# Kernel tuning notes

Hardware: AMD Instinct MI355X
Metric: run time of the kernel (lower is better)

The kernel has to match this reference:

```python
import jax, jax.numpy as jnp
import numpy as np

B, N, C, O, K, D = 32, 2048, 64, 64, 3, 16

def setup_inputs() -> dict:
    key = jax.random.key(0)
    ks = jax.random.split(key, 6)
    x = jax.random.normal(ks[0], (B, N, C), dtype=jnp.float32)
    node_embeddings = jax.random.normal(ks[1], (N, D), dtype=jnp.float32)
    adj_m = jax.random.uniform(ks[2], (N, N), dtype=jnp.float32)
    weights_pool = jax.random.normal(ks[3], (D, K, C, O), dtype=jnp.float32) * 0.1
    bias_pool = jax.random.normal(ks[4], (D, O), dtype=jnp.float32) * 0.1
    sa_weight = jax.random.normal(ks[5], (N, 2 * N), dtype=jnp.float32) * (1.0 / np.sqrt(2 * N))
    return {"x": x, "node_embeddings": node_embeddings, "adj_m": adj_m,
            "weights_pool": weights_pool, "bias_pool": bias_pool, "sa_weight": sa_weight}

def reference(x, node_embeddings, adj_m, weights_pool, bias_pool, sa_weight):
    n = node_embeddings.shape[0]
    # learned adaptive adjacency [N,N]
    supports = jax.nn.softmax(jax.nn.relu(node_embeddings @ node_embeddings.T), axis=1)
    # SpatialAttention: 1x1 conv over 2N channels == matmul with [N,2N] weight
    z = jnp.concatenate([supports, adj_m], axis=1) @ sa_weight.T  # [N,N]
    s2 = jax.nn.sigmoid(z)
    supports = s2 * adj_m + (1.0 - s2) * supports
    # Chebyshev polynomial basis
    support_set = [jnp.eye(n, dtype=supports.dtype), supports]
    for _ in range(2, K):
        support_set.append(2.0 * supports @ support_set[-1] - support_set[-2])
    supports_k = jnp.stack(support_set, axis=0)  # [K,N,N]
    # per-node generated weights/bias from embeddings
    weights = jnp.einsum('nd,dkio->nkio', node_embeddings, weights_pool)  # [N,K,C,O]
    bias = node_embeddings @ bias_pool  # [N,O]
    # graph conv: aggregate then per-node matmul
    x_g = jnp.einsum('knm,bmc->bnkc', supports_k, x)  # [B,N,K,C]
    x_gconv = jnp.einsum('bnki,nkio->bno', x_g, weights) + bias  # [B,N,O]
    return x_gconv
```

## Files before the change

### kernel.cpp

```cpp
#include <hip/hip_runtime.h>


typedef unsigned short u16;
typedef float f32x4 __attribute__((ext_vector_type(4)));
typedef __bf16 bf16x8 __attribute__((ext_vector_type(8)));
typedef unsigned short u16x8 __attribute__((ext_vector_type(8)));

__device__ __forceinline__ u16 f2bf(float f) {
    unsigned u = __float_as_uint(f);
    u += 0x7FFFu + ((u >> 16) & 1u);
    return (u16)(u >> 16);
}
__device__ __forceinline__ float bf2f(u16 h) {
    return __uint_as_float((unsigned)h << 16);
}
__device__ __forceinline__ void gl_lds16(const void* g, void* l) {
    __builtin_amdgcn_global_load_lds(
        (const __attribute__((address_space(1))) unsigned*)g,
        (__attribute__((address_space(3))) unsigned*)l, 16, 0, 0);
}

__global__ __launch_bounds__(256)
void supports_softmax(const float* __restrict__ E, u16* __restrict__ Acat) {
    const int n = blockIdx.x, tid = threadIdx.x;
    const int lane = tid & 63, wave = tid >> 6;
    __shared__ float red[4];
    float e[16];
#pragma unroll
    for (int d = 0; d < 16; ++d) e[d] = E[n * 16 + d];
    float v[8];
    float mx = 0.f;
#pragma unroll
    for (int r = 0; r < 8; ++r) {
        int m = r * 256 + tid;
        const float4* Er = (const float4*)(E + (size_t)m * 16);
        float4 a = Er[0], b = Er[1], c = Er[2], d4 = Er[3];
        float s = 0.f;
        s = fmaf(a.x, e[0], s);  s = fmaf(a.y, e[1], s);
        s = fmaf(a.z, e[2], s);  s = fmaf(a.w, e[3], s);
        s = fmaf(b.x, e[4], s);  s = fmaf(b.y, e[5], s);
        s = fmaf(b.z, e[6], s);  s = fmaf(b.w, e[7], s);
        s = fmaf(c.x, e[8], s);  s = fmaf(c.y, e[9], s);
        s = fmaf(c.z, e[10], s); s = fmaf(c.w, e[11], s);
        s = fmaf(d4.x, e[12], s); s = fmaf(d4.y, e[13], s);
        s = fmaf(d4.z, e[14], s); s = fmaf(d4.w, e[15], s);
        s = fmaxf(s, 0.f);
        v[r] = s;
        mx = fmaxf(mx, s);
    }
    for (int off = 32; off; off >>= 1) mx = fmaxf(mx, __shfl_down(mx, off, 64));
    if (lane == 0) red[wave] = mx;
    __syncthreads();
    mx = fmaxf(fmaxf(red[0], red[1]), fmaxf(red[2], red[3]));
    __syncthreads();
    float sum = 0.f;
#pragma unroll
    for (int r = 0; r < 8; ++r) { v[r] = __expf(v[r] - mx); sum += v[r]; }
    for (int off = 32; off; off >>= 1) sum += __shfl_down(sum, off, 64);
    if (lane == 0) red[wave] = sum;
    __syncthreads();
    sum = red[0] + red[1] + red[2] + red[3];
    float inv = 1.f / sum;
#pragma unroll
    for (int r = 0; r < 8; ++r)
        Acat[(size_t)n * 4096 + r * 256 + tid] = f2bf(v[r] * inv);
}

__global__ __launch_bounds__(256)
void cast_inputs(const float* __restrict__ adj, const float* __restrict__ saw,
                 const float* __restrict__ x, u16* __restrict__ Acat,
                 u16* __restrict__ sawb, u16* __restrict__ x_bf) {
    int bid = blockIdx.x;
    if (bid < 4096) {
        size_t j = ((size_t)bid * 256 + threadIdx.x) * 4;
        float4 v = *(const float4*)(adj + j);
        int n = (int)(j >> 11), c = (int)(j & 2047);
        ushort4 o = make_ushort4(f2bf(v.x), f2bf(v.y), f2bf(v.z), f2bf(v.w));
        *(ushort4*)(Acat + (size_t)n * 4096 + 2048 + c) = o;
    } else if (bid < 12288) {
        size_t j = ((size_t)(bid - 4096) * 256 + threadIdx.x) * 4;
        float4 v = *(const float4*)(saw + j);
        ushort4 o = make_ushort4(f2bf(v.x), f2bf(v.y), f2bf(v.z), f2bf(v.w));
        *(ushort4*)(sawb + j) = o;
    } else {
        size_t j = ((size_t)(bid - 12288) * 256 + threadIdx.x) * 4;
        float4 v = *(const float4*)(x + j);
        ushort4 o = make_ushort4(f2bf(v.x), f2bf(v.y), f2bf(v.z), f2bf(v.w));
        *(ushort4*)(x_bf + j) = o;
    }
}

__global__ __launch_bounds__(256)
void build_xtT(const float* __restrict__ x, u16* __restrict__ xtT) {
    __shared__ u16 t[64][65];
    int b = blockIdx.y, m0 = blockIdx.x * 64;
    int c = threadIdx.x & 63, g = threadIdx.x >> 6;
#pragma unroll
    for (int r = 0; r < 16; ++r) {
        int mm = g * 16 + r;
        t[mm][c] = f2bf(x[((size_t)b * 2048 + m0 + mm) * 64 + c]);
    }
    __syncthreads();
#pragma unroll
    for (int r = 0; r < 16; ++r) {
        int cc = g * 16 + r;
        xtT[((size_t)b * 64 + cc) * 2048 + m0 + c] = t[c][cc];
    }
}

__global__ __launch_bounds__(256, 3)
void gemm_bt(const u16* __restrict__ A, const u16* __restrict__ Bt,
             u16* __restrict__ Cp, int M, int N, int K, int Kh) {
    __shared__ alignas(16) u16 As[128 * 64];
    __shared__ alignas(16) u16 Bs[128 * 64];
    const int tid = threadIdx.x, lane = tid & 63, wave = tid >> 6;
    const int m0 = blockIdx.y * 128, n0 = blockIdx.x * 128;
    const int wm = (wave >> 1) * 64, wn = (wave & 1) * 64;
    const int kbeg = blockIdx.z * Kh, kend = kbeg + Kh;
    const int ml = lane & 15, c0l = lane >> 4;
    f32x4 acc[4][4] = {};

    int baseA[4], mskA[4], baseB[4], mskB[4];
#pragma unroll
    for (int i = 0; i < 4; ++i) { int m = wm + i * 16 + ml; baseA[i] = m * 8; mskA[i] = m & 7; }
#pragma unroll
    for (int j = 0; j < 4; ++j) { int nn = wn + j * 16 + ml; baseB[j] = nn * 8; mskB[j] = nn & 7; }

    for (int k0 = kbeg; k0 < kend; k0 += 64) {
#pragma unroll
        for (int r = 0; r < 4; ++r) {
            int s = wave * 64 + r * 256 + lane;
            int row = s >> 3, gc = (s & 7) ^ (row & 7);
            gl_lds16(A + (size_t)(m0 + row) * K + k0 + gc * 8, As + (size_t)s * 8);
        }
#pragma unroll
        for (int r = 0; r < 4; ++r) {
            int s = wave * 64 + r * 256 + lane;
            int row = s >> 3, gc = (s & 7) ^ (row & 7);
            gl_lds16(Bt + (size_t)(n0 + row) * K + k0 + gc * 8, Bs + (size_t)s * 8);
        }
        __syncthreads();
#pragma unroll
        for (int ks4 = 0; ks4 < 8; ks4 += 4) {
            bf16x8 af[4], bv[4];
#pragma unroll
            for (int i = 0; i < 4; ++i)
                af[i] = *(const bf16x8*)(As + (baseA[i] + ((c0l + ks4) ^ mskA[i])) * 8);
#pragma unroll
            for (int j = 0; j < 4; ++j)
                bv[j] = *(const bf16x8*)(Bs + (baseB[j] + ((c0l + ks4) ^ mskB[j])) * 8);
#pragma unroll
            for (int i = 0; i < 4; ++i)
#pragma unroll
                for (int j = 0; j < 4; ++j)
                    acc[i][j] = __builtin_amdgcn_mfma_f32_16x16x32_bf16(af[i], bv[j], acc[i][j], 0, 0, 0);
        }
        __syncthreads();
    }

    const int col_l = lane & 15, row_l = (lane >> 4) * 4;
    u16* Cz = Cp + (size_t)blockIdx.z * M * N;
#pragma unroll
    for (int i = 0; i < 4; ++i)
#pragma unroll
        for (int j = 0; j < 4; ++j)
#pragma unroll
            for (int r = 0; r < 4; ++r) {
                int row = m0 + wm + i * 16 + row_l + r;
                int col = n0 + wn + j * 16 + col_l;
                Cz[(size_t)row * N + col] = f2bf(acc[i][j][r]);
            }
}

#define PSTRIDE ((size_t)2048 * 2048)
__global__ __launch_bounds__(256)
void reduce_z(const u16* __restrict__ p, const float* __restrict__ adj,
              const u16* __restrict__ Acat, u16* __restrict__ S) {
    size_t j = ((size_t)blockIdx.x * 256 + threadIdx.x) * 4;
    ushort4 p0 = *(const ushort4*)(p + j);
    ushort4 p1 = *(const ushort4*)(p + PSTRIDE + j);
    ushort4 p2 = *(const ushort4*)(p + 2 * PSTRIDE + j);
    ushort4 p3 = *(const ushort4*)(p + 3 * PSTRIDE + j);
    float4 ad = *(const float4*)(adj + j);
    int row = (int)(j >> 11), col = (int)(j & 2047);
    ushort4 sp = *(const ushort4*)(Acat + (size_t)row * 4096 + col);
    float z0 = bf2f(p0.x) + bf2f(p1.x) + bf2f(p2.x) + bf2f(p3.x);
    float z1 = bf2f(p0.y) + bf2f(p1.y) + bf2f(p2.y) + bf2f(p3.y);
    float z2 = bf2f(p0.z) + bf2f(p1.z) + bf2f(p2.z) + bf2f(p3.z);
    float z3 = bf2f(p0.w) + bf2f(p1.w) + bf2f(p2.w) + bf2f(p3.w);
    float s0 = 1.f / (1.f + __expf(-z0)), s1 = 1.f / (1.f + __expf(-z1));
    float s2 = 1.f / (1.f + __expf(-z2)), s3 = 1.f / (1.f + __expf(-z3));
    ushort4 o = make_ushort4(
        f2bf(s0 * ad.x + (1.f - s0) * bf2f(sp.x)),
        f2bf(s1 * ad.y + (1.f - s1) * bf2f(sp.y)),
        f2bf(s2 * ad.z + (1.f - s2) * bf2f(sp.z)),
        f2bf(s3 * ad.w + (1.f - s3) * bf2f(sp.w)));
    *(ushort4*)(S + j) = o;
}

__global__ __launch_bounds__(256)
void reduceT(const u16* __restrict__ p, u16* __restrict__ xg1b,
             u16* __restrict__ xg1T) {
    __shared__ u16 t[64][65];
    int bx = blockIdx.x * 64, by = blockIdx.y * 64;
    int c = threadIdx.x & 63, g = threadIdx.x >> 6;
    int b = bx >> 6;
#pragma unroll
    for (int r = 0; r < 16; ++r) {
        int row = g * 16 + r;
        size_t idx = (size_t)(by + row) * 2048 + bx + c;
        u16 v = f2bf(bf2f(p[idx]) + bf2f(p[PSTRIDE + idx]) +
                     bf2f(p[2 * PSTRIDE + idx]) + bf2f(p[3 * PSTRIDE + idx]));
        xg1b[((size_t)b * 2048 + by + row) * 64 + c] = v;
        t[row][c] = v;
    }
    __syncthreads();
#pragma unroll
    for (int r = 0; r < 16; ++r) {
        int row = g * 16 + r;
        xg1T[(size_t)(bx + row) * 2048 + by + c] = t[c][row];
    }
}

__global__ __launch_bounds__(256)
void reduce2(const u16* __restrict__ p, u16* __restrict__ xg2b) {
    size_t j = ((size_t)blockIdx.x * 256 + threadIdx.x) * 4;
    ushort4 p0 = *(const ushort4*)(p + j);
    ushort4 p1 = *(const ushort4*)(p + PSTRIDE + j);
    ushort4 p2 = *(const ushort4*)(p + 2 * PSTRIDE + j);
    ushort4 p3 = *(const ushort4*)(p + 3 * PSTRIDE + j);
    int n = (int)(j >> 11), bc = (int)(j & 2047);
    int b = bc >> 6, c = bc & 63;
    ushort4 o = make_ushort4(
        f2bf(bf2f(p0.x) + bf2f(p1.x) + bf2f(p2.x) + bf2f(p3.x)),
        f2bf(bf2f(p0.y) + bf2f(p1.y) + bf2f(p2.y) + bf2f(p3.y)),
        f2bf(bf2f(p0.z) + bf2f(p1.z) + bf2f(p2.z) + bf2f(p3.z)),
        f2bf(bf2f(p0.w) + bf2f(p1.w) + bf2f(p2.w) + bf2f(p3.w)));
    *(ushort4*)(xg2b + ((size_t)b * 2048 + n) * 64 + c) = o;
}

__global__ __launch_bounds__(256)
void prep(const float* __restrict__ Wp, const float* __restrict__ E,
          const float* __restrict__ bp, u16* __restrict__ Wpb,
          float* __restrict__ bias) {
    const int bid = blockIdx.x, tid = threadIdx.x;
    if (bid < 16) {
        const int d = bid;
        const float* base = Wp + (size_t)d * 12288;
        for (int idx = tid; idx < 12288; idx += 256) {
            int o = idx / 192, ki = idx - o * 192;
            int k = ki >> 6, i = ki & 63;
            float v;
            if (k == 0)      v = base[i * 64 + o] - base[2 * 4096 + i * 64 + o];
            else if (k == 1) v = base[4096 + i * 64 + o];
            else             v = 2.f * base[2 * 4096 + i * 64 + o];
            Wpb[(size_t)(d * 64 + o) * 192 + ki] = f2bf(v);
        }
    } else {
        const int nb = bid - 16;
#pragma unroll
        for (int it = 0; it < 8; ++it) {
            int idx = tid + it * 256;
            int n = nb * 32 + (idx >> 6), o = idx & 63;
            float s = 0.f;
#pragma unroll
            for (int d = 0; d < 16; ++d) s = fmaf(E[n * 16 + d], bp[d * 64 + o], s);
            bias[(size_t)n * 64 + o] = s;
        }
    }
}

__global__ __launch_bounds__(256, 2)
void gconv_mfma(const u16* __restrict__ x_bf, const u16* __restrict__ xg1,
                const u16* __restrict__ xg2, const u16* __restrict__ Wpb,
                const float* __restrict__ bias, const float* __restrict__ E,
                float* __restrict__ out) {
    __shared__ alignas(16) u16 As[128 * 192];
    __shared__ alignas(16) u16 Bs[64 * 192];
    __shared__ float El[16 * 128];
    const int tid = threadIdx.x, lane = tid & 63, wave = tid >> 6;
    const int m0 = blockIdx.x * 128, nb = m0 & 2047;
    const int wm = (wave >> 1) * 64, wn = (wave & 1) * 32;
    const int ml = lane & 15, c0l = lane >> 4;
    const int col_l = lane & 15, rl = (lane >> 4) * 4;

#pragma unroll
    for (int it = 0; it < 12; ++it) {
        int s = tid + it * 256;
        int row = s / 24, sc = s - row * 24;
        int gc = (sc & 24) | ((sc ^ row) & 7);
        const u16* src = (gc < 8) ? x_bf : (gc < 16 ? xg1 : xg2);
        gl_lds16(src + (size_t)(m0 + row) * 64 + (gc & 7) * 8, As + (size_t)s * 8);
    }
#pragma unroll
    for (int it = 0; it < 8; ++it) {
        int idx = tid + it * 256;
        El[idx] = E[(size_t)(nb + (idx & 127)) * 16 + (idx >> 7)];
    }
    f32x4 oacc[4][2];
#pragma unroll
    for (int i = 0; i < 4; ++i)
#pragma unroll
        for (int j = 0; j < 2; ++j)
#pragma unroll
            for (int r = 0; r < 4; ++r)
                oacc[i][j][r] = bias[(size_t)(nb + wm + i * 16 + rl + r) * 64 + wn + j * 16 + col_l];
    __syncthreads();

    bf16x8 af[4][6];
#pragma unroll
    for (int i = 0; i < 4; ++i) {
        int m = wm + i * 16 + ml, base = m * 24, msk = m & 7;
#pragma unroll
        for (int ks = 0; ks < 6; ++ks) {
            int c = c0l + ks * 4;
            af[i][ks] = *(const bf16x8*)(As + (base + ((c & 24) | ((c ^ msk) & 7))) * 8);
        }
    }

    for (int d = 0; d < 16; ++d) {
        if (d) __syncthreads();
#pragma unroll
        for (int it = 0; it < 6; ++it) {
            int s = tid + it * 256;
            int row = s / 24, sc = s - row * 24;
            int gc = (sc & 24) | ((sc ^ row) & 7);
            gl_lds16(Wpb + (size_t)(d * 64 + row) * 192 + gc * 8, Bs + (size_t)s * 8);
        }
        __syncthreads();
        f32x4 tmp[4][2] = {};
#pragma unroll
        for (int ks = 0; ks < 6; ++ks) {
            bf16x8 bv[2];
#pragma unroll
            for (int j = 0; j < 2; ++j) {
                int o = wn + j * 16 + ml, msk = o & 7, c = c0l + ks * 4;
                bv[j] = *(const bf16x8*)(Bs + (o * 24 + ((c & 24) | ((c ^ msk) & 7))) * 8);
            }
#pragma unroll
            for (int i = 0; i < 4; ++i)
#pragma unroll
                for (int j = 0; j < 2; ++j)
                    tmp[i][j] = __builtin_amdgcn_mfma_f32_16x16x32_bf16(af[i][ks], bv[j], tmp[i][j], 0, 0, 0);
        }
#pragma unroll
        for (int i = 0; i < 4; ++i)
#pragma unroll
            for (int r = 0; r < 4; ++r) {
                float ev = El[d * 128 + wm + i * 16 + rl + r];
#pragma unroll
                for (int j = 0; j < 2; ++j)
                    oacc[i][j][r] = fmaf(ev, tmp[i][j][r], oacc[i][j][r]);
            }
    }
#pragma unroll
    for (int i = 0; i < 4; ++i)
#pragma unroll
        for (int j = 0; j < 2; ++j)
#pragma unroll
            for (int r = 0; r < 4; ++r)
                out[(size_t)(m0 + wm + i * 16 + rl + r) * 64 + wn + j * 16 + col_l] = oacc[i][j][r];
}

extern "C" void kernel_launch(void* const* d_in, const int* in_sizes, int n_in,
                              void* d_out, int out_size, void* d_ws, size_t ws_size,
                              hipStream_t stream) {
    const float* x   = (const float*)d_in[0];
    const float* E   = (const float*)d_in[1];
    const float* adj = (const float*)d_in[2];
    const float* Wp  = (const float*)d_in[3];
    const float* bp  = (const float*)d_in[4];
    const float* saw = (const float*)d_in[5];
    float* out = (float*)d_out;

    char* ws = (char*)d_ws;
    const size_t MB = 1u << 20;
    u16*   Acat  = (u16*)(ws);
    u16*   sawb  = (u16*)(ws + 16 * MB);
    u16*   XtT   = (u16*)(ws + 32 * MB);
    u16*   x_bf  = (u16*)(ws + 40 * MB);
    u16*   part  = (u16*)(ws + 48 * MB);
    u16*   S_bf  = (u16*)(ws + 16 * MB);
    u16*   xg1T  = (u16*)(ws + 24 * MB);
    u16*   xg1b  = (u16*)(ws);
    u16*   xg2b  = (u16*)(ws + 8 * MB);
    u16*   Wpb   = (u16*)(ws + 32 * MB);
    float* bias  = (float*)(ws + 33 * MB);

    supports_softmax<<<2048, 256, 0, stream>>>(E, Acat);
    cast_inputs<<<16384, 256, 0, stream>>>(adj, saw, x, Acat, sawb, x_bf);
    build_xtT<<<dim3(32, 32), 256, 0, stream>>>(x, XtT);

    gemm_bt<<<dim3(16, 16, 4), 256, 0, stream>>>(Acat, sawb, part, 2048, 2048, 4096, 1024);
    reduce_z<<<4096, 256, 0, stream>>>(part, adj, Acat, S_bf);
    gemm_bt<<<dim3(16, 16, 4), 256, 0, stream>>>(S_bf, XtT, part, 2048, 2048, 2048, 512);
    reduceT<<<dim3(32, 32), 256, 0, stream>>>(part, xg1b, xg1T);
    prep<<<80, 256, 0, stream>>>(Wp, E, bp, Wpb, bias);
    gemm_bt<<<dim3(16, 16, 4), 256, 0, stream>>>(S_bf, xg1T, part, 2048, 2048, 2048, 512);
    reduce2<<<4096, 256, 0, stream>>>(part, xg2b);

    gconv_mfma<<<512, 256, 0, stream>>>(x_bf, xg1b, xg2b, Wpb, bias, E, out);
}
```

Before: 306.2 us.

## Merge preprocessing kernels and fold split-K reduction and x cast into gconv

Merges softmax, casts, the x transpose and weight/bias prep into one preamble launch, and drops the separate x_bf cast. The reduce2 pass is removed: gconv_mfma now sums the four split-K partials and casts x to bf16 while loading its A tile, replacing async global-to-LDS loads with register loads. reduce_z reads the bf16 adjacency from Acat instead of the fp32 input, and reduceT is vectorized to ushort4 loads. The aim is fewer launches and less intermediate memory traffic, at the cost of losing the async LDS loads in gconv and using a slightly less precise adjacency blend.

```diff
diff --git a/kernel.cpp b/kernel.cpp
--- a/kernel.cpp
+++ b/kernel.cpp
@@ -6,6 +6,8 @@
 typedef __bf16 bf16x8 __attribute__((ext_vector_type(8)));
 typedef unsigned short u16x8 __attribute__((ext_vector_type(8)));
 
+#define PSTRIDE ((size_t)2048 * 2048)
+
 __device__ __forceinline__ u16 f2bf(float f) {
     unsigned u = __float_as_uint(f);
     u += 0x7FFFu + ((u >> 16) & 1u);
@@ -21,90 +23,109 @@
 }
 
 __global__ __launch_bounds__(256)
-void supports_softmax(const float* __restrict__ E, u16* __restrict__ Acat) {
-    const int n = blockIdx.x, tid = threadIdx.x;
-    const int lane = tid & 63, wave = tid >> 6;
+void preamble(const float* __restrict__ E, const float* __restrict__ adj,
+              const float* __restrict__ saw, const float* __restrict__ x,
+              const float* __restrict__ Wp, const float* __restrict__ bp,
+              u16* __restrict__ Acat, u16* __restrict__ sawb,
+              u16* __restrict__ xtT, u16* __restrict__ Wpb,
+              float* __restrict__ bias) {
     __shared__ float red[4];
-    float e[16];
-#pragma unroll
-    for (int d = 0; d < 16; ++d) e[d] = E[n * 16 + d];
-    float v[8];
-    float mx = 0.f;
-#pragma unroll
-    for (int r = 0; r < 8; ++r) {
-        int m = r * 256 + tid;
-        const float4* Er = (const float4*)(E + (size_t)m * 16);
-        float4 a = Er[0], b = Er[1], c = Er[2], d4 = Er[3];
-        float s = 0.f;
-        s = fmaf(a.x, e[0], s);  s = fmaf(a.y, e[1], s);
-        s = fmaf(a.z, e[2], s);  s = fmaf(a.w, e[3], s);
-        s = fmaf(b.x, e[4], s);  s = fmaf(b.y, e[5], s);
-        s = fmaf(b.z, e[6], s);  s = fmaf(b.w, e[7], s);
-        s = fmaf(c.x, e[8], s);  s = fmaf(c.y, e[9], s);
-        s = fmaf(c.z, e[10], s); s = fmaf(c.w, e[11], s);
-        s = fmaf(d4.x, e[12], s); s = fmaf(d4.y, e[13], s);
-        s = fmaf(d4.z, e[14], s); s = fmaf(d4.w, e[15], s);
-        s = fmaxf(s, 0.f);
-        v[r] = s;
-        mx = fmaxf(mx, s);
-    }
-    for (int off = 32; off; off >>= 1) mx = fmaxf(mx, __shfl_down(mx, off, 64));
-    if (lane == 0) red[wave] = mx;
-    __syncthreads();
-    mx = fmaxf(fmaxf(red[0], red[1]), fmaxf(red[2], red[3]));
-    __syncthreads();
-    float sum = 0.f;
-#pragma unroll
-    for (int r = 0; r < 8; ++r) { v[r] = __expf(v[r] - mx); sum += v[r]; }
-    for (int off = 32; off; off >>= 1) sum += __shfl_down(sum, off, 64);
-    if (lane == 0) red[wave] = sum;
-    __syncthreads();
-    sum = red[0] + red[1] + red[2] + red[3];
-    float inv = 1.f / sum;
-#pragma unroll
-    for (int r = 0; r < 8; ++r)
-        Acat[(size_t)n * 4096 + r * 256 + tid] = f2bf(v[r] * inv);
-}
-
-__global__ __launch_bounds__(256)
-void cast_inputs(const float* __restrict__ adj, const float* __restrict__ saw,
-                 const float* __restrict__ x, u16* __restrict__ Acat,
-                 u16* __restrict__ sawb, u16* __restrict__ x_bf) {
-    int bid = blockIdx.x;
-    if (bid < 4096) {
-        size_t j = ((size_t)bid * 256 + threadIdx.x) * 4;
+    __shared__ u16 t[64][65];
+    const int bid = blockIdx.x, tid = threadIdx.x;
+
+    if (bid < 2048) {
+        const int n = bid, lane = tid & 63, wave = tid >> 6;
+        float e[16];
+#pragma unroll
+        for (int d = 0; d < 16; ++d) e[d] = E[n * 16 + d];
+        float v[8];
+        float mx = 0.f;
+#pragma unroll
+        for (int r = 0; r < 8; ++r) {
+            int m = r * 256 + tid;
+            const float4* Er = (const float4*)(E + (size_t)m * 16);
+            float4 a = Er[0], b = Er[1], c = Er[2], d4 = Er[3];
+            float s = 0.f;
+            s = fmaf(a.x, e[0], s);  s = fmaf(a.y, e[1], s);
+            s = fmaf(a.z, e[2], s);  s = fmaf(a.w, e[3], s);
+            s = fmaf(b.x, e[4], s);  s = fmaf(b.y, e[5], s);
+            s = fmaf(b.z, e[6], s);  s = fmaf(b.w, e[7], s);
+            s = fmaf(c.x, e[8], s);  s = fmaf(c.y, e[9], s);
+            s = fmaf(c.z, e[10], s); s = fmaf(c.w, e[11], s);
+            s = fmaf(d4.x, e[12], s); s = fmaf(d4.y, e[13], s);
+            s = fmaf(d4.z, e[14], s); s = fmaf(d4.w, e[15], s);
+            s = fmaxf(s, 0.f);
+            v[r] = s;
+            mx = fmaxf(mx, s);
+        }
+        for (int off = 32; off; off >>= 1) mx = fmaxf(mx, __shfl_down(mx, off, 64));
+        if (lane == 0) red[wave] = mx;
+        __syncthreads();
+        mx = fmaxf(fmaxf(red[0], red[1]), fmaxf(red[2], red[3]));
+        __syncthreads();
+        float sum = 0.f;
+#pragma unroll
+        for (int r = 0; r < 8; ++r) { v[r] = __expf(v[r] - mx); sum += v[r]; }
+        for (int off = 32; off; off >>= 1) sum += __shfl_down(sum, off, 64);
+        if (lane == 0) red[wave] = sum;
+        __syncthreads();
+        sum = red[0] + red[1] + red[2] + red[3];
+        float inv = 1.f / sum;
+#pragma unroll
+        for (int r = 0; r < 8; ++r)
+            Acat[(size_t)n * 4096 + r * 256 + tid] = f2bf(v[r] * inv);
+    } else if (bid < 6144) {
+        size_t j = ((size_t)(bid - 2048) * 256 + tid) * 4;
         float4 v = *(const float4*)(adj + j);
         int n = (int)(j >> 11), c = (int)(j & 2047);
         ushort4 o = make_ushort4(f2bf(v.x), f2bf(v.y), f2bf(v.z), f2bf(v.w));
         *(ushort4*)(Acat + (size_t)n * 4096 + 2048 + c) = o;
-    } else if (bid < 12288) {
-        size_t j = ((size_t)(bid - 4096) * 256 + threadIdx.x) * 4;
+    } else if (bid < 14336) {
+        size_t j = ((size_t)(bid - 6144) * 256 + tid) * 4;
         float4 v = *(const float4*)(saw + j);
         ushort4 o = make_ushort4(f2bf(v.x), f2bf(v.y), f2bf(v.z), f2bf(v.w));
         *(ushort4*)(sawb + j) = o;
+    } else if (bid < 15360) {
+        int local = bid - 14336;
+        int m0 = (local & 31) * 64, b = local >> 5;
+        int c = tid & 63, g = tid >> 6;
+#pragma unroll
+        for (int r = 0; r < 16; ++r) {
+            int mm = g * 16 + r;
+            t[mm][c] = f2bf(x[((size_t)b * 2048 + m0 + mm) * 64 + c]);
+        }
+        __syncthreads();
+#pragma unroll
+        for (int r = 0; r < 16; ++r) {
+            int cc = g * 16 + r;
+            xtT[((size_t)b * 64 + cc) * 2048 + m0 + c] = t[c][cc];
+        }
     } else {
-        size_t j = ((size_t)(bid - 12288) * 256 + threadIdx.x) * 4;
-        float4 v = *(const float4*)(x + j);
-        ushort4 o = make_ushort4(f2bf(v.x), f2bf(v.y), f2bf(v.z), f2bf(v.w));
-        *(ushort4*)(x_bf + j) = o;
-    }
-}
-
-__global__ __launch_bounds__(256)
-void build_xtT(const float* __restrict__ x, u16* __restrict__ xtT) {
-    __shared__ u16 t[64][65];
-    int b = blockIdx.y, m0 = blockIdx.x * 64;
-    int c = threadIdx.x & 63, g = threadIdx.x >> 6;
-#pragma unroll
-    for (int r = 0; r < 16; ++r) {
-        int mm = g * 16 + r;
-        t[mm][c] = f2bf(x[((size_t)b * 2048 + m0 + mm) * 64 + c]);
-    }
-    __syncthreads();
-#pragma unroll
-    for (int r = 0; r < 16; ++r) {
-        int cc = g * 16 + r;
-        xtT[((size_t)b * 64 + cc) * 2048 + m0 + c] = t[c][cc];
+        int local = bid - 15360;
+        if (local < 16) {
+            const int d = local;
+            const float* base = Wp + (size_t)d * 12288;
+            for (int idx = tid; idx < 12288; idx += 256) {
+                int o = idx / 192, ki = idx - o * 192;
+                int k = ki >> 6, i = ki & 63;
+                float v;
+                if (k == 0)      v = base[i * 64 + o] - base[2 * 4096 + i * 64 + o];
+                else if (k == 1) v = base[4096 + i * 64 + o];
+                else             v = 2.f * base[2 * 4096 + i * 64 + o];
+                Wpb[(size_t)(d * 64 + o) * 192 + ki] = f2bf(v);
+            }
+        } else {
+            const int nb = local - 16;
+#pragma unroll
+            for (int it = 0; it < 8; ++it) {
+                int idx = tid + it * 256;
+                int n = nb * 32 + (idx >> 6), o = idx & 63;
+                float s = 0.f;
+#pragma unroll
+                for (int d = 0; d < 16; ++d) s = fmaf(E[n * 16 + d], bp[d * 64 + o], s);
+                bias[(size_t)n * 64 + o] = s;
+            }
+        }
     }
 }
 
@@ -172,18 +193,17 @@
             }
 }
 
-#define PSTRIDE ((size_t)2048 * 2048)
 __global__ __launch_bounds__(256)
-void reduce_z(const u16* __restrict__ p, const float* __restrict__ adj,
-              const u16* __restrict__ Acat, u16* __restrict__ S) {
+void reduce_z(const u16* __restrict__ p, const u16* __restrict__ Acat,
+              u16* __restrict__ S) {
     size_t j = ((size_t)blockIdx.x * 256 + threadIdx.x) * 4;
     ushort4 p0 = *(const ushort4*)(p + j);
     ushort4 p1 = *(const ushort4*)(p + PSTRIDE + j);
     ushort4 p2 = *(const ushort4*)(p + 2 * PSTRIDE + j);
     ushort4 p3 = *(const ushort4*)(p + 3 * PSTRIDE + j);
-    float4 ad = *(const float4*)(adj + j);
     int row = (int)(j >> 11), col = (int)(j & 2047);
     ushort4 sp = *(const ushort4*)(Acat + (size_t)row * 4096 + col);
+    ushort4 ad = *(const ushort4*)(Acat + (size_t)row * 4096 + 2048 + col);
     float z0 = bf2f(p0.x) + bf2f(p1.x) + bf2f(p2.x) + bf2f(p3.x);
     float z1 = bf2f(p0.y) + bf2f(p1.y) + bf2f(p2.y) + bf2f(p3.y);
     float z2 = bf2f(p0.z) + bf2f(p1.z) + bf2f(p2.z) + bf2f(p3.z);
@@ -191,30 +211,38 @@
     float s0 = 1.f / (1.f + __expf(-z0)), s1 = 1.f / (1.f + __expf(-z1));
     float s2 = 1.f / (1.f + __expf(-z2)), s3 = 1.f / (1.f + __expf(-z3));
     ushort4 o = make_ushort4(
-        f2bf(s0 * ad.x + (1.f - s0) * bf2f(sp.x)),
-        f2bf(s1 * ad.y + (1.f - s1) * bf2f(sp.y)),
-        f2bf(s2 * ad.z + (1.f - s2) * bf2f(sp.z)),
-        f2bf(s3 * ad.w + (1.f - s3) * bf2f(sp.w)));
+        f2bf(s0 * bf2f(ad.x) + (1.f - s0) * bf2f(sp.x)),
+        f2bf(s1 * bf2f(ad.y) + (1.f - s1) * bf2f(sp.y)),
+        f2bf(s2 * bf2f(ad.z) + (1.f - s2) * bf2f(sp.z)),
+        f2bf(s3 * bf2f(ad.w) + (1.f - s3) * bf2f(sp.w)));
     *(ushort4*)(S + j) = o;
 }
 
 __global__ __launch_bounds__(256)
 void reduceT(const u16* __restrict__ p, u16* __restrict__ xg1b,
              u16* __restrict__ xg1T) {
-    __shared__ u16 t[64][65];
+    __shared__ u16 t[64][68];
     int bx = blockIdx.x * 64, by = blockIdx.y * 64;
+    int cg = threadIdx.x & 15, rg = threadIdx.x >> 4;
+    int b = bx >> 6;
+#pragma unroll
+    for (int rr = 0; rr < 4; ++rr) {
+        int row = rg * 4 + rr;
+        size_t idx = (size_t)(by + row) * 2048 + bx + cg * 4;
+        ushort4 q0 = *(const ushort4*)(p + idx);
+        ushort4 q1 = *(const ushort4*)(p + PSTRIDE + idx);
+        ushort4 q2 = *(const ushort4*)(p + 2 * PSTRIDE + idx);
+        ushort4 q3 = *(const ushort4*)(p + 3 * PSTRIDE + idx);
+        ushort4 v = make_ushort4(
+            f2bf(bf2f(q0.x) + bf2f(q1.x) + bf2f(q2.x) + bf2f(q3.x)),
+            f2bf(bf2f(q0.y) + bf2f(q1.y) + bf2f(q2.y) + bf2f(q3.y)),
+            f2bf(bf2f(q0.z) + bf2f(q1.z) + bf2f(q2.z) + bf2f(q3.z)),
+            f2bf(bf2f(q0.w) + bf2f(q1.w) + bf2f(q2.w) + bf2f(q3.w)));
+        *(ushort4*)(xg1b + ((size_t)b * 2048 + by + row) * 64 + cg * 4) = v;
+        *(ushort4*)(&t[row][cg * 4]) = v;
+    }
+    __syncthreads();
     int c = threadIdx.x & 63, g = threadIdx.x >> 6;
-    int b = bx >> 6;
-#pragma unroll
-    for (int r = 0; r < 16; ++r) {
-        int row = g * 16 + r;
-        size_t idx = (size_t)(by + row) * 2048 + bx + c;
-        u16 v = f2bf(bf2f(p[idx]) + bf2f(p[PSTRIDE + idx]) +
-                     bf2f(p[2 * PSTRIDE + idx]) + bf2f(p[3 * PSTRIDE + idx]));
-        xg1b[((size_t)b * 2048 + by + row) * 64 + c] = v;
-        t[row][c] = v;
-    }
-    __syncthreads();
 #pragma unroll
     for (int r = 0; r < 16; ++r) {
         int row = g * 16 + r;
@@ -222,64 +250,16 @@
     }
 }
 
-__global__ __launch_bounds__(256)
-void reduce2(const u16* __restrict__ p, u16* __restrict__ xg2b) {
-    size_t j = ((size_t)blockIdx.x * 256 + threadIdx.x) * 4;
-    ushort4 p0 = *(const ushort4*)(p + j);
-    ushort4 p1 = *(const ushort4*)(p + PSTRIDE + j);
-    ushort4 p2 = *(const ushort4*)(p + 2 * PSTRIDE + j);
-    ushort4 p3 = *(const ushort4*)(p + 3 * PSTRIDE + j);
-    int n = (int)(j >> 11), bc = (int)(j & 2047);
-    int b = bc >> 6, c = bc & 63;
-    ushort4 o = make_ushort4(
-        f2bf(bf2f(p0.x) + bf2f(p1.x) + bf2f(p2.x) + bf2f(p3.x)),
-        f2bf(bf2f(p0.y) + bf2f(p1.y) + bf2f(p2.y) + bf2f(p3.y)),
-        f2bf(bf2f(p0.z) + bf2f(p1.z) + bf2f(p2.z) + bf2f(p3.z)),
-        f2bf(bf2f(p0.w) + bf2f(p1.w) + bf2f(p2.w) + bf2f(p3.w)));
-    *(ushort4*)(xg2b + ((size_t)b * 2048 + n) * 64 + c) = o;
-}
-
-__global__ __launch_bounds__(256)
-void prep(const float* __restrict__ Wp, const float* __restrict__ E,
-          const float* __restrict__ bp, u16* __restrict__ Wpb,
-          float* __restrict__ bias) {
-    const int bid = blockIdx.x, tid = threadIdx.x;
-    if (bid < 16) {
-        const int d = bid;
-        const float* base = Wp + (size_t)d * 12288;
-        for (int idx = tid; idx < 12288; idx += 256) {
-            int o = idx / 192, ki = idx - o * 192;
-            int k = ki >> 6, i = ki & 63;
-            float v;
-            if (k == 0)      v = base[i * 64 + o] - base[2 * 4096 + i * 64 + o];
-            else if (k == 1) v = base[4096 + i * 64 + o];
-            else             v = 2.f * base[2 * 4096 + i * 64 + o];
-            Wpb[(size_t)(d * 64 + o) * 192 + ki] = f2bf(v);
-        }
-    } else {
-        const int nb = bid - 16;
-#pragma unroll
-        for (int it = 0; it < 8; ++it) {
-            int idx = tid + it * 256;
-            int n = nb * 32 + (idx >> 6), o = idx & 63;
-            float s = 0.f;
-#pragma unroll
-            for (int d = 0; d < 16; ++d) s = fmaf(E[n * 16 + d], bp[d * 64 + o], s);
-            bias[(size_t)n * 64 + o] = s;
-        }
-    }
-}
-
 __global__ __launch_bounds__(256, 2)
-void gconv_mfma(const u16* __restrict__ x_bf, const u16* __restrict__ xg1,
-                const u16* __restrict__ xg2, const u16* __restrict__ Wpb,
+void gconv_mfma(const float* __restrict__ x, const u16* __restrict__ xg1,
+                const u16* __restrict__ p, const u16* __restrict__ Wpb,
                 const float* __restrict__ bias, const float* __restrict__ E,
                 float* __restrict__ out) {
     __shared__ alignas(16) u16 As[128 * 192];
     __shared__ alignas(16) u16 Bs[64 * 192];
     __shared__ float El[16 * 128];
     const int tid = threadIdx.x, lane = tid & 63, wave = tid >> 6;
-    const int m0 = blockIdx.x * 128, nb = m0 & 2047;
+    const int m0 = blockIdx.x * 128, nb = m0 & 2047, bB = m0 >> 11;
     const int wm = (wave >> 1) * 64, wn = (wave & 1) * 32;
     const int ml = lane & 15, c0l = lane >> 4;
     const int col_l = lane & 15, rl = (lane >> 4) * 4;
@@ -289,8 +269,27 @@
         int s = tid + it * 256;
         int row = s / 24, sc = s - row * 24;
         int gc = (sc & 24) | ((sc ^ row) & 7);
-        const u16* src = (gc < 8) ? x_bf : (gc < 16 ? xg1 : xg2);
-        gl_lds16(src + (size_t)(m0 + row) * 64 + (gc & 7) * 8, As + (size_t)s * 8);
+        int grow = m0 + row;
+        u16x8 v;
+        if (gc < 8) {
+            const float* xp = x + (size_t)grow * 64 + gc * 8;
+            float4 a = *(const float4*)xp, b4 = *(const float4*)(xp + 4);
+            v[0] = f2bf(a.x);  v[1] = f2bf(a.y);  v[2] = f2bf(a.z);  v[3] = f2bf(a.w);
+            v[4] = f2bf(b4.x); v[5] = f2bf(b4.y); v[6] = f2bf(b4.z); v[7] = f2bf(b4.w);
+        } else if (gc < 16) {
+            v = *(const u16x8*)(xg1 + (size_t)grow * 64 + (gc & 7) * 8);
+        } else {
+            int n = grow & 2047, c8 = (gc & 7) * 8;
+            const u16* pp = p + (size_t)n * 2048 + bB * 64 + c8;
+            u16x8 q0 = *(const u16x8*)pp;
+            u16x8 q1 = *(const u16x8*)(pp + PSTRIDE);
+            u16x8 q2 = *(const u16x8*)(pp + 2 * PSTRIDE);
+            u16x8 q3 = *(const u16x8*)(pp + 3 * PSTRIDE);
+#pragma unroll
+            for (int tt = 0; tt < 8; ++tt)
+                v[tt] = f2bf(bf2f(q0[tt]) + bf2f(q1[tt]) + bf2f(q2[tt]) + bf2f(q3[tt]));
+        }
+        *(u16x8*)(As + (size_t)s * 8) = v;
     }
 #pragma unroll
     for (int it = 0; it < 8; ++it) {
@@ -378,26 +377,20 @@
     u16*   Acat  = (u16*)(ws);
     u16*   sawb  = (u16*)(ws + 16 * MB);
     u16*   XtT   = (u16*)(ws + 32 * MB);
-    u16*   x_bf  = (u16*)(ws + 40 * MB);
+    u16*   Wpb   = (u16*)(ws + 40 * MB);
+    float* bias  = (float*)(ws + 41 * MB);
     u16*   part  = (u16*)(ws + 48 * MB);
     u16*   S_bf  = (u16*)(ws + 16 * MB);
     u16*   xg1T  = (u16*)(ws + 24 * MB);
     u16*   xg1b  = (u16*)(ws);
-    u16*   xg2b  = (u16*)(ws + 8 * MB);
-    u16*   Wpb   = (u16*)(ws + 32 * MB);
-    float* bias  = (float*)(ws + 33 * MB);
-
-    supports_softmax<<<2048, 256, 0, stream>>>(E, Acat);
-    cast_inputs<<<16384, 256, 0, stream>>>(adj, saw, x, Acat, sawb, x_bf);
-    build_xtT<<<dim3(32, 32), 256, 0, stream>>>(x, XtT);
+
+    preamble<<<15440, 256, 0, stream>>>(E, adj, saw, x, Wp, bp, Acat, sawb, XtT, Wpb, bias);
 
     gemm_bt<<<dim3(16, 16, 4), 256, 0, stream>>>(Acat, sawb, part, 2048, 2048, 4096, 1024);
-    reduce_z<<<4096, 256, 0, stream>>>(part, adj, Acat, S_bf);
+    reduce_z<<<4096, 256, 0, stream>>>(part, Acat, S_bf);
     gemm_bt<<<dim3(16, 16, 4), 256, 0, stream>>>(S_bf, XtT, part, 2048, 2048, 2048, 512);
     reduceT<<<dim3(32, 32), 256, 0, stream>>>(part, xg1b, xg1T);
-    prep<<<80, 256, 0, stream>>>(Wp, E, bp, Wpb, bias);
     gemm_bt<<<dim3(16, 16, 4), 256, 0, stream>>>(S_bf, xg1T, part, 2048, 2048, 2048, 512);
-    reduce2<<<4096, 256, 0, stream>>>(part, xg2b);
-
-    gconv_mfma<<<512, 256, 0, stream>>>(x_bf, xg1b, xg2b, Wpb, bias, E, out);
-}
+
+    gconv_mfma<<<512, 256, 0, stream>>>(x, xg1b, part, Wpb, bias, E, out);
+}
```

After: 288.1 us. 5.9% less time.
